# Kernel optimization log

Hardware: AMD Instinct MI355X
Metric: run time of the kernel (lower is better)

Reference implementation:

```python
import jax, jax.numpy as jnp
import numpy as np

BT, P, C = 64, 1024, 1024   # bt = B*T with T=8 frames
T = 8
B = BT // T
RANK, DSTATE = 32, 16
SCALING = 128.0 / 32.0      # alpha / rank


def setup_inputs() -> dict:
    key = jax.random.key(0)
    ks = jax.random.split(key, 11)
    s = 0.02
    return {
        "x": jax.random.normal(ks[0], (BT, P, C), jnp.float32),
        "Wb": jax.random.normal(ks[1], (C, C), jnp.float32) * s,
        "bb": jax.random.normal(ks[2], (C,), jnp.float32) * s,
        "Wdown": jax.random.normal(ks[3], (RANK, C), jnp.float32) * s,
        "Wup": jax.random.normal(ks[4], (C, RANK), jnp.float32) * s,
        "A_log": jax.random.normal(ks[5], (RANK, DSTATE), jnp.float32),
        "Dp": jax.random.normal(ks[6], (RANK,), jnp.float32),
        "Wxp": jax.random.normal(ks[7], (RANK + 2 * DSTATE, RANK), jnp.float32) * s,
        "bxp": jnp.zeros((RANK + 2 * DSTATE,), jnp.float32),
        "Wout": jax.random.normal(ks[8], (RANK, RANK), jnp.float32) * s,
        "bout": jnp.zeros((RANK,), jnp.float32),
    }


def _minimal_ssm(xseq, A_log, Dp, Wxp, bxp, Wout, bout):
    # xseq: (N, T, r) -> (N, T, r); serial recurrence over T via lax.scan.
    N, Tn, r = xseq.shape
    A = -jnp.exp(A_log)  # (r, s)

    def step(h, x_t):  # h: (N, r, s), x_t: (N, r)
        proj = x_t @ Wxp.T + bxp                      # (N, r + 2s)
        dlt = jax.nn.softplus(proj[:, :r])            # (N, r)
        Bm = proj[:, r:r + DSTATE]                    # (N, s)
        Cm = proj[:, r + DSTATE:]                     # (N, s)
        A_bar = jnp.exp(dlt[:, :, None] * A)          # (N, r, s)
        B_bar = dlt[:, :, None] * Bm[:, None, :]      # (N, r, s)
        h = A_bar * h + B_bar * x_t[:, :, None]
        y = jnp.einsum('nrs,ns->nr', h, Cm) + Dp * x_t
        return h, y

    h0 = jnp.zeros((N, r, DSTATE), xseq.dtype)
    _, ys = jax.lax.scan(step, h0, jnp.swapaxes(xseq, 0, 1))  # ys: (T, N, r)
    out = jnp.swapaxes(ys, 0, 1)                               # (N, T, r)
    return out @ Wout.T + bout


def reference(x, Wb, bb, Wdown, Wup, A_log, Dp, Wxp, bxp, Wout, bout):
    base_out = x @ Wb.T + bb                                   # (BT, P, C)
    x_btpc = x.reshape(B, T, P, C)
    red = jnp.einsum('btpc,rc->btpr', x_btpc, Wdown)           # (B, T, P, r)
    red_seq = jnp.transpose(red, (0, 2, 1, 3)).reshape(B * P, T, RANK)
    red_seq = _minimal_ssm(red_seq, A_log, Dp, Wxp, bxp, Wout, bout)
    red_seq = jnp.transpose(red_seq.reshape(B, P, T, RANK), (0, 2, 1, 3))
    delta = jnp.einsum('btpr,cr->btpc', red_seq, Wup) * SCALING
    return base_out + delta.reshape(BT, P, C)
```

## Files before the change

### kernel.cpp

```cpp
#include <hip/hip_runtime.h>
#include <stdint.h>

typedef unsigned short u16;
typedef short short8 __attribute__((ext_vector_type(8)));
typedef float f32x4 __attribute__((ext_vector_type(4)));

#define MFMA16(a,b,c) __builtin_amdgcn_mfma_f32_16x16x32_bf16((a),(b),(c),0,0,0)

__device__ __forceinline__ u16 f2bf(float f) {
  union { float f; unsigned u; } v; v.f = f;
  unsigned r = v.u + 0x7FFFu + ((v.u >> 16) & 1u);
  return (u16)(r >> 16);
}

__device__ __forceinline__ void async16(u16* lds, const u16* g) {
  __builtin_amdgcn_global_load_lds(
      (const __attribute__((address_space(1))) void*)g,
      (__attribute__((address_space(3))) void*)lds, 16, 0, 0);
}

__global__ __launch_bounds__(256) void k_conv_x(const float* __restrict__ x,
                                                u16* __restrict__ xb, int n8) {
  int stride = gridDim.x * blockDim.x;
  for (int i = blockIdx.x * blockDim.x + threadIdx.x; i < n8; i += stride) {
    const float4* p = (const float4*)(x + (size_t)i * 8);
    float4 a = p[0], b = p[1];
    union { u16 h[8]; uint4 v; } o;
    o.h[0] = f2bf(a.x); o.h[1] = f2bf(a.y); o.h[2] = f2bf(a.z); o.h[3] = f2bf(a.w);
    o.h[4] = f2bf(b.x); o.h[5] = f2bf(b.y); o.h[6] = f2bf(b.z); o.h[7] = f2bf(b.w);
    *(uint4*)(xb + (size_t)i * 8) = o.v;
  }
}

__global__ __launch_bounds__(256) void k_conv_w(const float* __restrict__ wb,
                                                const float* __restrict__ wdown,
                                                const float* __restrict__ wup,
                                                u16* __restrict__ wbb,
                                                u16* __restrict__ wdownb,
                                                u16* __restrict__ wupb) {
  int idx = blockIdx.x * blockDim.x + threadIdx.x;
  int total = gridDim.x * blockDim.x;
  for (int i = idx; i < 1024 * 1024 / 8; i += total) {
    const float4* p = (const float4*)(wb + (size_t)i * 8);
    float4 a = p[0], b = p[1];
    union { u16 h[8]; uint4 v; } o;
    o.h[0] = f2bf(a.x); o.h[1] = f2bf(a.y); o.h[2] = f2bf(a.z); o.h[3] = f2bf(a.w);
    o.h[4] = f2bf(b.x); o.h[5] = f2bf(b.y); o.h[6] = f2bf(b.z); o.h[7] = f2bf(b.w);
    *(uint4*)(wbb + (size_t)i * 8) = o.v;
  }
  for (int i = idx; i < 32 * 1024; i += total) wdownb[i] = f2bf(wdown[i]);
  for (int i = idx; i < 1024 * 32; i += total) wupb[i] = f2bf(wup[i] * 4.0f);
}

__global__ __launch_bounds__(256) void k_red(const u16* __restrict__ xb,
                                             const u16* __restrict__ wdownb,
                                             float* __restrict__ red) {
  __shared__ u16 As[128 * 64];
  int tid = threadIdx.x;
  int lane = tid & 63, wid = tid >> 6;
  int m0 = blockIdx.x * 128;
  f32x4 acc[2][2] = {};
  int srow = wid * 32 + (lane >> 3);
  int scol = (lane & 7) * 8;
  const u16* gA = xb + (size_t)(m0 + srow) * 1024 + scol;
  u16* lA = &As[(wid * 32) * 64];
  for (int k0 = 0; k0 < 1024; k0 += 64) {
    if (k0) __syncthreads();
    async16(lA,           gA + k0);
    async16(lA + 8 * 64,  gA + k0 + (size_t)8 * 1024);
    async16(lA + 16 * 64, gA + k0 + (size_t)16 * 1024);
    async16(lA + 24 * 64, gA + k0 + (size_t)24 * 1024);
    __syncthreads();
#pragma unroll
    for (int ks = 0; ks < 2; ++ks) {
      short8 a[2], b[2];
#pragma unroll
      for (int mi = 0; mi < 2; ++mi)
        a[mi] = *(const short8*)&As[(wid * 32 + mi * 16 + (lane & 15)) * 64 +
                                    ks * 32 + (lane >> 4) * 8];
#pragma unroll
      for (int ni = 0; ni < 2; ++ni)
        b[ni] = *(const short8*)(wdownb + (size_t)(ni * 16 + (lane & 15)) * 1024 +
                                 k0 + ks * 32 + (lane >> 4) * 8);
#pragma unroll
      for (int mi = 0; mi < 2; ++mi)
#pragma unroll
        for (int ni = 0; ni < 2; ++ni)
          acc[mi][ni] = MFMA16(a[mi], b[ni], acc[mi][ni]);
    }
  }
#pragma unroll
  for (int mi = 0; mi < 2; ++mi)
#pragma unroll
    for (int ni = 0; ni < 2; ++ni)
#pragma unroll
      for (int r = 0; r < 4; ++r) {
        int row = m0 + wid * 32 + mi * 16 + (lane >> 4) * 4 + r;
        int col = ni * 16 + (lane & 15);
        red[(size_t)row * 32 + col] = acc[mi][ni][r];
      }
}

__global__ __launch_bounds__(256) void k_ssm(const float* __restrict__ red,
                                             u16* __restrict__ oseq,
                                             const float* __restrict__ A_log,
                                             const float* __restrict__ Dp,
                                             const float* __restrict__ Wxp,
                                             const float* __restrict__ bxp,
                                             const float* __restrict__ Wout,
                                             const float* __restrict__ bout) {
  __shared__ float sx[8][32], sbc[8][32], sy[8][32];
  int tid = threadIdx.x;
  int g = tid >> 5, r = tid & 31;
  int n = blockIdx.x * 8 + g;
  int b = n >> 10, p = n & 1023;
  float wxA[32], wxB[32], wo[32];
#pragma unroll
  for (int k = 0; k < 32; ++k) {
    wxA[k] = Wxp[r * 32 + k];
    wxB[k] = Wxp[(32 + r) * 32 + k];
    wo[k]  = Wout[r * 32 + k];
  }
  float Ar[16];
#pragma unroll
  for (int s = 0; s < 16; ++s) Ar[s] = -__expf(A_log[r * 16 + s]);
  float dpr = Dp[r];
  float bx1 = bxp[r], bx2 = bxp[32 + r], bo = bout[r];
  float h[16];
#pragma unroll
  for (int s = 0; s < 16; ++s) h[s] = 0.f;
  for (int t = 0; t < 8; ++t) {
    size_t rowt = (size_t)(b * 8 + t) * 1024 + p;
    float xr = red[rowt * 32 + r];
    sx[g][r] = xr;
    __syncthreads();
    float p1 = bx1, p2 = bx2;
#pragma unroll
    for (int k = 0; k < 32; ++k) {
      float xv = sx[g][k];
      p1 = fmaf(wxA[k], xv, p1);
      p2 = fmaf(wxB[k], xv, p2);
    }
    float dlt = (p1 > 20.f) ? p1 : log1pf(__expf(p1));
    sbc[g][r] = p2;
    __syncthreads();
    float yr = dpr * xr;
#pragma unroll
    for (int s = 0; s < 16; ++s) {
      float Bm = sbc[g][s];
      float Cm = sbc[g][16 + s];
      float ab = __expf(dlt * Ar[s]);
      h[s] = fmaf(ab, h[s], dlt * Bm * xr);
      yr = fmaf(h[s], Cm, yr);
    }
    sy[g][r] = yr;
    __syncthreads();
    float ov = bo;
#pragma unroll
    for (int k = 0; k < 32; ++k) ov = fmaf(wo[k], sy[g][k], ov);
    oseq[rowt * 32 + r] = f2bf(ov);
  }
}

__global__ __launch_bounds__(256) void k_gemm(const u16* __restrict__ xb,
                                              const u16* __restrict__ wbb,
                                              const u16* __restrict__ oseq,
                                              const u16* __restrict__ wupb,
                                              const float* __restrict__ bb,
                                              float* __restrict__ out) {
  __shared__ u16 As[128 * 32];
  __shared__ u16 Bs[128 * 32];
  int bid = blockIdx.x;
  int sw = (bid & 7) * 512 + (bid >> 3);
  int mt = sw >> 3, nt = sw & 7;
  int m0 = mt * 128, n0 = nt * 128;
  int tid = threadIdx.x, lane = tid & 63, wid = tid >> 6;
  int wr = (wid >> 1) * 64, wc = (wid & 1) * 64;
  f32x4 acc[4][4] = {};
  int srow = wid * 32 + (lane >> 2);
  int scol = (lane & 3) * 8;
  const u16* gA = xb  + (size_t)(m0 + srow) * 1024 + scol;
  const u16* gB = wbb + (size_t)(n0 + srow) * 1024 + scol;
  u16* lA = &As[wid * 32 * 32];
  u16* lB = &Bs[wid * 32 * 32];
  for (int k0 = 0; k0 < 1024; k0 += 32) {
    if (k0) __syncthreads();
    async16(lA,           gA + k0);
    async16(lA + 16 * 32, gA + k0 + (size_t)16 * 1024);
    async16(lB,           gB + k0);
    async16(lB + 16 * 32, gB + k0 + (size_t)16 * 1024);
    __syncthreads();
    short8 a[4], b[4];
#pragma unroll
    for (int mi = 0; mi < 4; ++mi)
      a[mi] = *(const short8*)&As[(wr + mi * 16 + (lane & 15)) * 32 + (lane >> 4) * 8];
#pragma unroll
    for (int ni = 0; ni < 4; ++ni)
      b[ni] = *(const short8*)&Bs[(wc + ni * 16 + (lane & 15)) * 32 + (lane >> 4) * 8];
#pragma unroll
    for (int mi = 0; mi < 4; ++mi)
#pragma unroll
      for (int ni = 0; ni < 4; ++ni)
        acc[mi][ni] = MFMA16(a[mi], b[ni], acc[mi][ni]);
  }
  short8 ae[4], be[4];
#pragma unroll
  for (int mi = 0; mi < 4; ++mi) {
    int row = m0 + wr + mi * 16 + (lane & 15);
    ae[mi] = *(const short8*)(oseq + (size_t)row * 32 + (lane >> 4) * 8);
  }
#pragma unroll
  for (int ni = 0; ni < 4; ++ni) {
    int col = n0 + wc + ni * 16 + (lane & 15);
    be[ni] = *(const short8*)(wupb + (size_t)col * 32 + (lane >> 4) * 8);
  }
#pragma unroll
  for (int mi = 0; mi < 4; ++mi)
#pragma unroll
    for (int ni = 0; ni < 4; ++ni)
      acc[mi][ni] = MFMA16(ae[mi], be[ni], acc[mi][ni]);
  float bias[4];
#pragma unroll
  for (int ni = 0; ni < 4; ++ni) bias[ni] = bb[n0 + wc + ni * 16 + (lane & 15)];
#pragma unroll
  for (int mi = 0; mi < 4; ++mi)
#pragma unroll
    for (int ni = 0; ni < 4; ++ni) {
      int col = n0 + wc + ni * 16 + (lane & 15);
#pragma unroll
      for (int r = 0; r < 4; ++r) {
        int row = m0 + wr + mi * 16 + (lane >> 4) * 4 + r;
        out[(size_t)row * 1024 + col] = acc[mi][ni][r] + bias[ni];
      }
    }
}

extern "C" void kernel_launch(void* const* d_in, const int* in_sizes, int n_in,
                              void* d_out, int out_size, void* d_ws, size_t ws_size,
                              hipStream_t stream) {
  const float* x     = (const float*)d_in[0];
  const float* Wb    = (const float*)d_in[1];
  const float* bb    = (const float*)d_in[2];
  const float* Wdown = (const float*)d_in[3];
  const float* Wup   = (const float*)d_in[4];
  const float* A_log = (const float*)d_in[5];
  const float* Dp    = (const float*)d_in[6];
  const float* Wxp   = (const float*)d_in[7];
  const float* bxp   = (const float*)d_in[8];
  const float* Wout  = (const float*)d_in[9];
  const float* bout  = (const float*)d_in[10];

  char* ws = (char*)d_ws;
  u16*   xb     = (u16*)(ws);
  u16*   wbb    = (u16*)(ws + 134217728);
  u16*   wdownb = (u16*)(ws + 136314880);
  u16*   wupb   = (u16*)(ws + 136380416);
  float* red    = (float*)(ws + 136445952);
  u16*   oseq   = (u16*)(ws + 144834560);
  float* out = (float*)d_out;

  hipLaunchKernelGGL(k_conv_x, dim3(8192), dim3(256), 0, stream, x, xb, 64 * 1024 * 1024 / 8);
  hipLaunchKernelGGL(k_conv_w, dim3(512), dim3(256), 0, stream, Wb, Wdown, Wup, wbb, wdownb, wupb);
  hipLaunchKernelGGL(k_red, dim3(512), dim3(256), 0, stream, xb, wdownb, red);
  hipLaunchKernelGGL(k_ssm, dim3(1024), dim3(256), 0, stream, red, oseq, A_log, Dp, Wxp, bxp, Wout, bout);
  hipLaunchKernelGGL(k_gemm, dim3(4096), dim3(256), 0, stream, xb, wbb, oseq, wupb, bb, out);
}
```

Before: 688.8 us.

## Fuse x bf16 conversion with down-projection GEMM; use shuffles in SSM

Merges the fp32-to-bf16 conversion of x with the rank-32 down-projection so that x is read once in fp32, converted in registers, written as bf16 and fed straight into MFMA. This removes a separate kernel launch and a full re-read of the 128 MB bf16 copy of x. The SSM kernel also replaces shared-memory exchanges and block-wide barriers with wavefront shuffles, putting two sequences in each wave. The fused kernel relies on direct global loads rather than LDS staging, which may leave some memory latency less well hidden.

Result: no change. 686.7 us (-0.3%).

```diff
diff --git a/kernel.cpp b/kernel.cpp
--- a/kernel.cpp
+++ b/kernel.cpp
@@ -17,19 +17,6 @@
   __builtin_amdgcn_global_load_lds(
       (const __attribute__((address_space(1))) void*)g,
       (__attribute__((address_space(3))) void*)lds, 16, 0, 0);
-}
-
-__global__ __launch_bounds__(256) void k_conv_x(const float* __restrict__ x,
-                                                u16* __restrict__ xb, int n8) {
-  int stride = gridDim.x * blockDim.x;
-  for (int i = blockIdx.x * blockDim.x + threadIdx.x; i < n8; i += stride) {
-    const float4* p = (const float4*)(x + (size_t)i * 8);
-    float4 a = p[0], b = p[1];
-    union { u16 h[8]; uint4 v; } o;
-    o.h[0] = f2bf(a.x); o.h[1] = f2bf(a.y); o.h[2] = f2bf(a.z); o.h[3] = f2bf(a.w);
-    o.h[4] = f2bf(b.x); o.h[5] = f2bf(b.y); o.h[6] = f2bf(b.z); o.h[7] = f2bf(b.w);
-    *(uint4*)(xb + (size_t)i * 8) = o.v;
-  }
 }
 
 __global__ __launch_bounds__(256) void k_conv_w(const float* __restrict__ wb,
@@ -52,53 +39,37 @@
   for (int i = idx; i < 1024 * 32; i += total) wupb[i] = f2bf(wup[i] * 4.0f);
 }
 
-__global__ __launch_bounds__(256) void k_red(const u16* __restrict__ xb,
-                                             const u16* __restrict__ wdownb,
-                                             float* __restrict__ red) {
-  __shared__ u16 As[128 * 64];
-  int tid = threadIdx.x;
-  int lane = tid & 63, wid = tid >> 6;
-  int m0 = blockIdx.x * 128;
-  f32x4 acc[2][2] = {};
-  int srow = wid * 32 + (lane >> 3);
-  int scol = (lane & 7) * 8;
-  const u16* gA = xb + (size_t)(m0 + srow) * 1024 + scol;
-  u16* lA = &As[(wid * 32) * 64];
-  for (int k0 = 0; k0 < 1024; k0 += 64) {
-    if (k0) __syncthreads();
-    async16(lA,           gA + k0);
-    async16(lA + 8 * 64,  gA + k0 + (size_t)8 * 1024);
-    async16(lA + 16 * 64, gA + k0 + (size_t)16 * 1024);
-    async16(lA + 24 * 64, gA + k0 + (size_t)24 * 1024);
-    __syncthreads();
-#pragma unroll
-    for (int ks = 0; ks < 2; ++ks) {
-      short8 a[2], b[2];
-#pragma unroll
-      for (int mi = 0; mi < 2; ++mi)
-        a[mi] = *(const short8*)&As[(wid * 32 + mi * 16 + (lane & 15)) * 64 +
-                                    ks * 32 + (lane >> 4) * 8];
-#pragma unroll
-      for (int ni = 0; ni < 2; ++ni)
-        b[ni] = *(const short8*)(wdownb + (size_t)(ni * 16 + (lane & 15)) * 1024 +
-                                 k0 + ks * 32 + (lane >> 4) * 8);
-#pragma unroll
-      for (int mi = 0; mi < 2; ++mi)
-#pragma unroll
-        for (int ni = 0; ni < 2; ++ni)
-          acc[mi][ni] = MFMA16(a[mi], b[ni], acc[mi][ni]);
-    }
-  }
-#pragma unroll
-  for (int mi = 0; mi < 2; ++mi)
-#pragma unroll
-    for (int ni = 0; ni < 2; ++ni)
-#pragma unroll
-      for (int r = 0; r < 4; ++r) {
-        int row = m0 + wid * 32 + mi * 16 + (lane >> 4) * 4 + r;
-        int col = ni * 16 + (lane & 15);
-        red[(size_t)row * 32 + col] = acc[mi][ni][r];
-      }
+__global__ __launch_bounds__(256) void k_prep(const float* __restrict__ x,
+                                              const u16* __restrict__ wdownb,
+                                              u16* __restrict__ xb,
+                                              float* __restrict__ red) {
+  int lane = threadIdx.x & 63, wid = threadIdx.x >> 6;
+  int base = blockIdx.x * 64 + wid * 16;
+  int row = base + (lane & 15);
+  int q8 = (lane >> 4) * 8;
+  const float* gx = x + (size_t)row * 1024 + q8;
+  u16* gxb = xb + (size_t)row * 1024 + q8;
+  const u16* wd0 = wdownb + (size_t)(lane & 15) * 1024 + q8;
+  f32x4 acc0 = {}, acc1 = {};
+#pragma unroll 4
+  for (int k0 = 0; k0 < 1024; k0 += 32) {
+    float4 a = *(const float4*)(gx + k0);
+    float4 c = *(const float4*)(gx + k0 + 4);
+    union { u16 h[8]; uint4 v; short8 s; } o;
+    o.h[0] = f2bf(a.x); o.h[1] = f2bf(a.y); o.h[2] = f2bf(a.z); o.h[3] = f2bf(a.w);
+    o.h[4] = f2bf(c.x); o.h[5] = f2bf(c.y); o.h[6] = f2bf(c.z); o.h[7] = f2bf(c.w);
+    *(uint4*)(gxb + k0) = o.v;
+    short8 b0 = *(const short8*)(wd0 + k0);
+    short8 b1 = *(const short8*)(wd0 + k0 + 16 * 1024);
+    acc0 = MFMA16(o.s, b0, acc0);
+    acc1 = MFMA16(o.s, b1, acc1);
+  }
+  int orow = base + (lane >> 4) * 4;
+#pragma unroll
+  for (int rr = 0; rr < 4; ++rr) {
+    red[(size_t)(orow + rr) * 32 + (lane & 15)] = acc0[rr];
+    red[(size_t)(orow + rr) * 32 + 16 + (lane & 15)] = acc1[rr];
+  }
 }
 
 __global__ __launch_bounds__(256) void k_ssm(const float* __restrict__ red,
@@ -109,10 +80,11 @@
                                              const float* __restrict__ bxp,
                                              const float* __restrict__ Wout,
                                              const float* __restrict__ bout) {
-  __shared__ float sx[8][32], sbc[8][32], sy[8][32];
-  int tid = threadIdx.x;
-  int g = tid >> 5, r = tid & 31;
-  int n = blockIdx.x * 8 + g;
+  int lane = threadIdx.x & 63;
+  int r = lane & 31;
+  int hb = lane & 32;
+  int gw = blockIdx.x * 4 + (threadIdx.x >> 6);
+  int n = gw * 2 + (lane >> 5);
   int b = n >> 10, p = n & 1023;
   float wxA[32], wxB[32], wo[32];
 #pragma unroll
@@ -132,32 +104,26 @@
   for (int t = 0; t < 8; ++t) {
     size_t rowt = (size_t)(b * 8 + t) * 1024 + p;
     float xr = red[rowt * 32 + r];
-    sx[g][r] = xr;
-    __syncthreads();
     float p1 = bx1, p2 = bx2;
 #pragma unroll
     for (int k = 0; k < 32; ++k) {
-      float xv = sx[g][k];
+      float xv = __shfl(xr, hb + k);
       p1 = fmaf(wxA[k], xv, p1);
       p2 = fmaf(wxB[k], xv, p2);
     }
     float dlt = (p1 > 20.f) ? p1 : log1pf(__expf(p1));
-    sbc[g][r] = p2;
-    __syncthreads();
     float yr = dpr * xr;
 #pragma unroll
     for (int s = 0; s < 16; ++s) {
-      float Bm = sbc[g][s];
-      float Cm = sbc[g][16 + s];
+      float Bm = __shfl(p2, hb + s);
+      float Cm = __shfl(p2, hb + 16 + s);
       float ab = __expf(dlt * Ar[s]);
       h[s] = fmaf(ab, h[s], dlt * Bm * xr);
       yr = fmaf(h[s], Cm, yr);
     }
-    sy[g][r] = yr;
-    __syncthreads();
     float ov = bo;
 #pragma unroll
-    for (int k = 0; k < 32; ++k) ov = fmaf(wo[k], sy[g][k], ov);
+    for (int k = 0; k < 32; ++k) ov = fmaf(wo[k], __shfl(yr, hb + k), ov);
     oseq[rowt * 32 + r] = f2bf(ov);
   }
 }
@@ -259,9 +225,8 @@
   u16*   oseq   = (u16*)(ws + 144834560);
   float* out = (float*)d_out;
 
-  hipLaunchKernelGGL(k_conv_x, dim3(8192), dim3(256), 0, stream, x, xb, 64 * 1024 * 1024 / 8);
   hipLaunchKernelGGL(k_conv_w, dim3(512), dim3(256), 0, stream, Wb, Wdown, Wup, wbb, wdownb, wupb);
-  hipLaunchKernelGGL(k_red, dim3(512), dim3(256), 0, stream, xb, wdownb, red);
+  hipLaunchKernelGGL(k_prep, dim3(1024), dim3(256), 0, stream, x, wdownb, xb, red);
   hipLaunchKernelGGL(k_ssm, dim3(1024), dim3(256), 0, stream, red, oseq, A_log, Dp, Wxp, bxp, Wout, bout);
   hipLaunchKernelGGL(k_gemm, dim3(4096), dim3(256), 0, stream, xb, wbb, oseq, wupb, bb, out);
 }
```
